# Kernel tuning notes

Hardware: AMD Instinct MI355X
Metric: run time of the kernel (lower is better)

Reference implementation:

```python
import jax, jax.numpy as jnp
import numpy as np

B, L, H = 32, 2048, 512


def setup_inputs() -> dict:
    key = jax.random.key(0)
    k1, k2, k3, k4, k5, k6 = jax.random.split(key, 6)
    scale = 1.0 / np.sqrt(H)
    return {
        "query": jax.random.normal(k1, (B, H), dtype=jnp.float32),
        "ref": jax.random.normal(k2, (B, L, H), dtype=jnp.float32),
        "mask": jax.random.randint(k3, (B, L), 0, 2) == 1,
        # learned params (torch Linear weight layout: [out, in]; apply as x @ W.T)
        "W_ref": jax.random.normal(k4, (H, H), dtype=jnp.float32) * scale,
        "W_q": jax.random.normal(k5, (H, H), dtype=jnp.float32) * scale,
        "v": jax.random.normal(k6, (H,), dtype=jnp.float32) * scale,
    }


def reference(query, ref, mask, W_ref, W_q, v):
    scale = 1.0 / np.sqrt(H)
    # additive (Bahdanau) scores: v^T tanh(W_ref ref + W_q q)
    encoded_ref = jnp.einsum("blh,oh->blo", ref, W_ref)          # (B, L, H)
    encoded_q = jnp.einsum("bh,oh->bo", query, W_q)[:, None, :]  # (B, 1, H)
    scores = jnp.einsum("blh,h->bl", jnp.tanh(encoded_ref + encoded_q), v)
    scores = scores * scale
    scores = jnp.where(mask, -1e9, scores)
    attn = jax.nn.softmax(scores, axis=1)                         # (B, L)
    glimpse = jnp.einsum("bl,blh->bh", attn, ref)                 # (B, H)
    return glimpse, scores
```

## Files before the change

### kernel.cpp

```cpp
#include <hip/hip_runtime.h>
#include <hip/hip_bf16.h>
#include <cstdint>

typedef __attribute__((ext_vector_type(4))) float f32x4;
typedef __attribute__((ext_vector_type(8))) short s16x8;

#define NB   32
#define NL   2048
#define NH   512
#define NM   (NB * NL)
#define SCALE 0.04419417382415922f

__device__ __forceinline__ ushort f2bf(float f) {
    __hip_bfloat16 b = __float2bfloat16(f);
    return *reinterpret_cast<ushort*>(&b);
}
__device__ __forceinline__ float bf2f(unsigned u) {
    union { unsigned u; float f; } a; a.u = u << 16; return a.f;
}
__device__ __forceinline__ unsigned long long pack4(float4 f) {
    union { ushort u[4]; unsigned long long v; } p;
    p.u[0] = f2bf(f.x); p.u[1] = f2bf(f.y); p.u[2] = f2bf(f.z); p.u[3] = f2bf(f.w);
    return p.v;
}

#define GL16(g, l)                                                         \
    __builtin_amdgcn_global_load_lds(                                      \
        (const __attribute__((address_space(1))) unsigned int*)(g),        \
        (__attribute__((address_space(3))) unsigned int*)(l), 16, 0, 0)

__global__ __launch_bounds__(256) void k_conv(const float* __restrict__ ref,
                                              ushort* __restrict__ refb,
                                              const float* __restrict__ W,
                                              ushort* __restrict__ Wb,
                                              const float* __restrict__ query,
                                              const float* __restrict__ Wq,
                                              float* __restrict__ eq) {
    int bid = blockIdx.x;
    int t = threadIdx.x;
    if (bid < 32768) {
        int g = bid * 256 + t;
        ((unsigned long long*)refb)[g] = pack4(((const float4*)ref)[g]);
    } else if (bid < 33024) {
        int g = (bid - 32768) * 256 + t;
        ((unsigned long long*)Wb)[g] = pack4(((const float4*)W)[g]);
    } else {
        __shared__ float q[NH];
        int b = bid - 33024;
        q[t] = query[b * NH + t];
        q[t + 256] = query[b * NH + t + 256];
        __syncthreads();
#pragma unroll
        for (int half = 0; half < 2; ++half) {
            int o = t + half * 256;
            const float4* w = (const float4*)(Wq + (size_t)o * NH);
            float acc = 0.f;
#pragma unroll 4
            for (int i = 0; i < NH / 4; ++i) {
                float4 x = w[i];
                acc += q[4 * i] * x.x + q[4 * i + 1] * x.y + q[4 * i + 2] * x.z + q[4 * i + 3] * x.w;
            }
            eq[b * NH + o] = acc;
        }
    }
}

__global__ __launch_bounds__(512, 1) void k_gemm8(const ushort* __restrict__ refb,
                                                  const ushort* __restrict__ Wb,
                                                  const float* __restrict__ eq,
                                                  const float* __restrict__ v,
                                                  float* __restrict__ part) {
    __shared__ ushort smem[65536];
    ushort* As0 = smem;
    ushort* Bs0 = smem + 16384;
    ushort* As1 = smem + 32768;
    ushort* Bs1 = smem + 49152;

    int tid = threadIdx.x;
    int lane = tid & 63, wid = tid >> 6;
    int wr = wid >> 2, wc = wid & 3;

    int phys = blockIdx.x;
    int xcd = phys & 7, slot = phys >> 3;
    int mt = xcd * 32 + (slot >> 1);
    int nt = slot & 1;
    int m0g = mt << 8, n0 = nt << 8;
    int b = mt >> 3;

    f32x4 acc[8][4];
#pragma unroll
    for (int i = 0; i < 8; ++i)
#pragma unroll
        for (int j = 0; j < 4; ++j) acc[i][j] = (f32x4)(0.f);

    int lr = lane & 15, kq = lane >> 4;
    int l7 = lr & 7;
    int sA0 = ((kq) ^ l7) << 3;
    int sA1 = ((4 + kq) ^ l7) << 3;
    int abase0 = (wr * 128 + lr) * 64;
    int bbase0 = (wc * 64 + lr) * 64;

#define STAGE(Asb, Bsb, kt)                                                    \
    {   _Pragma("unroll")                                                      \
        for (int ho = 0; ho < 4; ++ho) {                                       \
            int br = (ho >> 1) * 128 + wid * 16 + (ho & 1) * 8;                \
            int rl = br + (lane >> 3);                                         \
            int gc = (lane & 7) ^ (rl & 7);                                    \
            GL16(refb + (size_t)(m0g + rl) * NH + (kt) * 64 + gc * 8, (Asb) + br * 64); \
            GL16(Wb   + (size_t)(n0  + rl) * NH + (kt) * 64 + gc * 8, (Bsb) + br * 64); \
        } }

#define TILE_BODY(Asb, Bsb)                                                    \
    {   s16x8 bq[4][2];                                                        \
        _Pragma("unroll")                                                      \
        for (int fc = 0; fc < 4; ++fc) {                                       \
            bq[fc][0] = *(const s16x8*)&(Bsb)[bbase0 + fc * 1024 + sA0];       \
            bq[fc][1] = *(const s16x8*)&(Bsb)[bbase0 + fc * 1024 + sA1];       \
        }                                                                      \
        __builtin_amdgcn_s_setprio(1);                                         \
        _Pragma("unroll")                                                      \
        for (int fr = 0; fr < 8; ++fr) {                                       \
            s16x8 a0 = *(const s16x8*)&(Asb)[abase0 + fr * 1024 + sA0];        \
            s16x8 a1 = *(const s16x8*)&(Asb)[abase0 + fr * 1024 + sA1];        \
            _Pragma("unroll")                                                  \
            for (int fc = 0; fc < 4; ++fc) {                                   \
                acc[fr][fc] = __builtin_amdgcn_mfma_f32_16x16x32_bf16(         \
                    a0, bq[fc][0], acc[fr][fc], 0, 0, 0);                      \
                acc[fr][fc] = __builtin_amdgcn_mfma_f32_16x16x32_bf16(         \
                    a1, bq[fc][1], acc[fr][fc], 0, 0, 0);                      \
            }                                                                  \
        }                                                                      \
        __builtin_amdgcn_s_setprio(0);                                         \
    }

#define TILE(Asb, Bsb, WAITN, DOSTAGE, Asn, Bsn, kstage)                       \
    {   asm volatile("s_waitcnt vmcnt(" #WAITN ")" ::: "memory");              \
        __builtin_amdgcn_s_barrier();                                          \
        TILE_BODY(Asb, Bsb)                                                    \
        asm volatile("s_waitcnt lgkmcnt(0)" ::: "memory");                     \
        __builtin_amdgcn_s_barrier();                                          \
        if (DOSTAGE) STAGE(Asn, Bsn, kstage)                                   \
    }

    STAGE(As0, Bs0, 0)
    STAGE(As1, Bs1, 1)

    TILE(As0, Bs0, 8, 1, As0, Bs0, 2)
    TILE(As1, Bs1, 8, 1, As1, Bs1, 3)
    TILE(As0, Bs0, 8, 1, As0, Bs0, 4)
    TILE(As1, Bs1, 8, 1, As1, Bs1, 5)
    TILE(As0, Bs0, 8, 1, As0, Bs0, 6)
    TILE(As1, Bs1, 8, 1, As1, Bs1, 7)
    TILE(As0, Bs0, 8, 0, As0, Bs0, 0)
    TILE(As1, Bs1, 0, 0, As1, Bs1, 0)

#undef STAGE
#undef TILE_BODY
#undef TILE

    __syncthreads();

    float* sc_red = (float*)smem;
    const float* eqb = eq + b * NH;
    float vv[4], ee[4];
#pragma unroll
    for (int fc = 0; fc < 4; ++fc) {
        int c = n0 + wc * 64 + fc * 16 + lr;
        vv[fc] = v[c];
        ee[fc] = eqb[c];
    }
#pragma unroll
    for (int fr = 0; fr < 8; ++fr) {
#pragma unroll
        for (int reg = 0; reg < 4; ++reg) {
            float s = 0.f;
#pragma unroll
            for (int fc = 0; fc < 4; ++fc) {
                float x = acc[fr][fc][reg] + ee[fc];
                float t = 1.f - 2.f / (__expf(2.f * x) + 1.f);
                s += vv[fc] * t;
            }
            s += __shfl_xor(s, 1);
            s += __shfl_xor(s, 2);
            s += __shfl_xor(s, 4);
            s += __shfl_xor(s, 8);
            if (lr == 0) sc_red[wid * 128 + fr * 16 + kq * 4 + reg] = s;
        }
    }
    __syncthreads();
    if (tid < 256) {
        int row = tid;
        int g0 = (row >> 7) * 4;
        int rl = row & 127;
        float s = sc_red[(g0 + 0) * 128 + rl] + sc_red[(g0 + 1) * 128 + rl]
                + sc_red[(g0 + 2) * 128 + rl] + sc_red[(g0 + 3) * 128 + rl];
        part[(size_t)nt * NM + m0g + row] = s;
    }
}

__global__ __launch_bounds__(256) void k_smglp(const float* __restrict__ part,
                                               const int* __restrict__ mask,
                                               const ushort* __restrict__ refb,
                                               float* __restrict__ out_sc,
                                               float* __restrict__ glp) {
    int sp = blockIdx.x, b = blockIdx.y;
    int tid = threadIdx.x;
    int lane = tid & 63, wid = tid >> 6;
    __shared__ float red[4];
    __shared__ float asl[128];
    float sc[8];
    float mx = -3.4e38f;
#pragma unroll
    for (int i = 0; i < 8; ++i) {
        int m = b * NL + i * 256 + tid;
        float s = (part[m] + part[NM + m]) * SCALE;
        if (mask[m] != 0) s = -1e9f;
        if (sp == 0) out_sc[m] = s;
        sc[i] = s;
        mx = fmaxf(mx, s);
    }
#pragma unroll
    for (int o = 32; o >= 1; o >>= 1) mx = fmaxf(mx, __shfl_xor(mx, o));
    if (lane == 0) red[wid] = mx;
    __syncthreads();
    mx = fmaxf(fmaxf(red[0], red[1]), fmaxf(red[2], red[3]));
    __syncthreads();
    float ls = 0.f;
#pragma unroll
    for (int i = 0; i < 8; ++i) {
        float e = __expf(sc[i] - mx);
        ls += e;
        if (i == (sp >> 1) && (tid >> 7) == (sp & 1)) asl[tid & 127] = e;
    }
#pragma unroll
    for (int o = 32; o >= 1; o >>= 1) ls += __shfl_xor(ls, o);
    if (lane == 0) red[wid] = ls;
    __syncthreads();
    float inv = 1.f / (red[0] + red[1] + red[2] + red[3]);

    const ushort* rb = refb + ((size_t)b * NL + sp * 128) * NH;
    float2 acc = make_float2(0.f, 0.f);
#pragma unroll 4
    for (int l = 0; l < 128; ++l) {
        float a = asl[l];
        unsigned r = ((const unsigned*)(rb + (size_t)l * NH))[tid];
        acc.x += a * bf2f(r & 0xFFFFu);
        acc.y += a * bf2f(r >> 16);
    }
    acc.x *= inv;
    acc.y *= inv;
    ((float2*)(glp + (size_t)(sp * NB + b) * NH))[tid] = acc;
}

__global__ __launch_bounds__(256) void k_gred(const float* __restrict__ glp,
                                              float* __restrict__ out_gl) {
    int idx = blockIdx.x * 256 + threadIdx.x;
    float s = 0.f;
#pragma unroll
    for (int sp = 0; sp < 16; ++sp) s += glp[sp * (NB * NH) + idx];
    out_gl[idx] = s;
}

extern "C" void kernel_launch(void* const* d_in, const int* in_sizes, int n_in,
                              void* d_out, int out_size, void* d_ws, size_t ws_size,
                              hipStream_t stream) {
    const float* query = (const float*)d_in[0];
    const float* ref   = (const float*)d_in[1];
    const int*   mask  = (const int*)d_in[2];
    const float* W_ref = (const float*)d_in[3];
    const float* W_q   = (const float*)d_in[4];
    const float* v     = (const float*)d_in[5];

    float* out_gl = (float*)d_out;
    float* out_sc = out_gl + NB * NH;

    char* w = (char*)d_ws;
    ushort* wW   = (ushort*)w;
    float*  eq   = (float*)(w + 524288);
    ushort* refb = (ushort*)(w + 589824);
    float*  part = (float*)(w + 589824 + 67108864);
    float*  glp  = (float*)(w + 589824 + 67108864 + 524288);

    k_conv<<<33056, 256, 0, stream>>>(ref, refb, W_ref, wW, query, W_q, eq);
    k_gemm8<<<512, 512, 0, stream>>>(refb, wW, eq, v, part);
    k_smglp<<<dim3(16, NB), 256, 0, stream>>>(part, mask, refb, out_sc, glp);
    k_gred<<<64, 256, 0, stream>>>(glp, out_gl);
}
```

Baseline: 130.4 us.

## Fuse ref bf16 conversion into GEMM A-tile staging and read fp32 ref for glimpse

Drops the standalone pass that converted the full ref tensor to bf16. The GEMM now loads fp32 ref into registers, converts it, and writes swizzled bf16 into LDS while W tiles still use async global-to-LDS loads. The glimpse reduction reads fp32 ref directly. This removes a large write/read round trip through the workspace, at the cost of register-staged A loads with more VGPR pressure and doubled A bytes per GEMM load.

```diff
diff --git a/kernel.cpp b/kernel.cpp
--- a/kernel.cpp
+++ b/kernel.cpp
@@ -15,9 +15,6 @@
     __hip_bfloat16 b = __float2bfloat16(f);
     return *reinterpret_cast<ushort*>(&b);
 }
-__device__ __forceinline__ float bf2f(unsigned u) {
-    union { unsigned u; float f; } a; a.u = u << 16; return a.f;
-}
 __device__ __forceinline__ unsigned long long pack4(float4 f) {
     union { ushort u[4]; unsigned long long v; } p;
     p.u[0] = f2bf(f.x); p.u[1] = f2bf(f.y); p.u[2] = f2bf(f.z); p.u[3] = f2bf(f.w);
@@ -29,24 +26,25 @@
         (const __attribute__((address_space(1))) unsigned int*)(g),        \
         (__attribute__((address_space(3))) unsigned int*)(l), 16, 0, 0)
 
-__global__ __launch_bounds__(256) void k_conv(const float* __restrict__ ref,
-                                              ushort* __restrict__ refb,
-                                              const float* __restrict__ W,
-                                              ushort* __restrict__ Wb,
-                                              const float* __restrict__ query,
-                                              const float* __restrict__ Wq,
-                                              float* __restrict__ eq) {
+__global__ __launch_bounds__(256) void k_pre(const float* __restrict__ W,
+                                             ushort* __restrict__ Wb,
+                                             const float* __restrict__ query,
+                                             const float* __restrict__ Wq,
+                                             float* __restrict__ eq) {
     int bid = blockIdx.x;
     int t = threadIdx.x;
-    if (bid < 32768) {
-        int g = bid * 256 + t;
-        ((unsigned long long*)refb)[g] = pack4(((const float4*)ref)[g]);
-    } else if (bid < 33024) {
-        int g = (bid - 32768) * 256 + t;
-        ((unsigned long long*)Wb)[g] = pack4(((const float4*)W)[g]);
+    if (bid < 64) {
+        const float4* F = (const float4*)W;
+        unsigned long long* U = (unsigned long long*)Wb;
+        int base = bid * 1024 + t;
+        float4 f[4];
+#pragma unroll
+        for (int k = 0; k < 4; ++k) f[k] = F[base + k * 256];
+#pragma unroll
+        for (int k = 0; k < 4; ++k) U[base + k * 256] = pack4(f[k]);
     } else {
         __shared__ float q[NH];
-        int b = bid - 33024;
+        int b = bid - 64;
         q[t] = query[b * NH + t];
         q[t + 256] = query[b * NH + t + 256];
         __syncthreads();
@@ -65,7 +63,7 @@
     }
 }
 
-__global__ __launch_bounds__(512, 1) void k_gemm8(const ushort* __restrict__ refb,
+__global__ __launch_bounds__(512, 1) void k_gemm8(const float* __restrict__ ref,
                                                   const ushort* __restrict__ Wb,
                                                   const float* __restrict__ eq,
                                                   const float* __restrict__ v,
@@ -100,14 +98,30 @@
     int abase0 = (wr * 128 + lr) * 64;
     int bbase0 = (wc * 64 + lr) * 64;
 
-#define STAGE(Asb, Bsb, kt)                                                    \
+    const float* aglob = ref + (size_t)(m0g + wid * 32 + (lane >> 4)) * NH + (lane & 15) * 4;
+    float4 qa[8];
+
+#define STAGE_A(kt)                                                            \
+    {   _Pragma("unroll")                                                      \
+        for (int j = 0; j < 8; ++j)                                            \
+            qa[j] = *(const float4*)(aglob + (size_t)(j * 4) * NH + (kt) * 64); }
+
+#define WRITE_A(Asb)                                                           \
+    {   int s_ = lane & 15;                                                    \
+        _Pragma("unroll")                                                      \
+        for (int j = 0; j < 8; ++j) {                                          \
+            int rowj = wid * 32 + (lane >> 4) + j * 4;                         \
+            int idx = rowj * 64 + ((((s_ >> 1) ^ (rowj & 7))) << 3) + ((s_ & 1) << 2); \
+            *(unsigned long long*)&(Asb)[idx] = pack4(qa[j]);                  \
+        } }
+
+#define STAGE_B(Bsb, kt)                                                       \
     {   _Pragma("unroll")                                                      \
         for (int ho = 0; ho < 4; ++ho) {                                       \
-            int br = (ho >> 1) * 128 + wid * 16 + (ho & 1) * 8;                \
+            int br = wid * 32 + ho * 8;                                        \
             int rl = br + (lane >> 3);                                         \
             int gc = (lane & 7) ^ (rl & 7);                                    \
-            GL16(refb + (size_t)(m0g + rl) * NH + (kt) * 64 + gc * 8, (Asb) + br * 64); \
-            GL16(Wb   + (size_t)(n0  + rl) * NH + (kt) * 64 + gc * 8, (Bsb) + br * 64); \
+            GL16(Wb + (size_t)(n0 + rl) * NH + (kt) * 64 + gc * 8, (Bsb) + br * 64); \
         } }
 
 #define TILE_BODY(Asb, Bsb)                                                    \
@@ -133,30 +147,42 @@
         __builtin_amdgcn_s_setprio(0);                                         \
     }
 
-#define TILE(Asb, Bsb, WAITN, DOSTAGE, Asn, Bsn, kstage)                       \
-    {   asm volatile("s_waitcnt vmcnt(" #WAITN ")" ::: "memory");              \
-        __builtin_amdgcn_s_barrier();                                          \
-        TILE_BODY(Asb, Bsb)                                                    \
-        asm volatile("s_waitcnt lgkmcnt(0)" ::: "memory");                     \
-        __builtin_amdgcn_s_barrier();                                          \
-        if (DOSTAGE) STAGE(Asn, Bsn, kstage)                                   \
-    }
-
-    STAGE(As0, Bs0, 0)
-    STAGE(As1, Bs1, 1)
-
-    TILE(As0, Bs0, 8, 1, As0, Bs0, 2)
-    TILE(As1, Bs1, 8, 1, As1, Bs1, 3)
-    TILE(As0, Bs0, 8, 1, As0, Bs0, 4)
-    TILE(As1, Bs1, 8, 1, As1, Bs1, 5)
-    TILE(As0, Bs0, 8, 1, As0, Bs0, 6)
-    TILE(As1, Bs1, 8, 1, As1, Bs1, 7)
-    TILE(As0, Bs0, 8, 0, As0, Bs0, 0)
-    TILE(As1, Bs1, 0, 0, As1, Bs1, 0)
-
-#undef STAGE
+#define ENTRY(N)                                                               \
+    asm volatile("s_waitcnt lgkmcnt(0)" ::: "memory");                         \
+    asm volatile("s_waitcnt vmcnt(" #N ")" ::: "memory");                      \
+    __builtin_amdgcn_s_barrier();
+
+#define EXIT()                                                                 \
+    asm volatile("s_waitcnt lgkmcnt(0)" ::: "memory");                         \
+    __builtin_amdgcn_s_barrier();
+
+    STAGE_A(0) STAGE_B(Bs0, 0)
+    asm volatile("s_waitcnt vmcnt(4)" ::: "memory");
+    WRITE_A(As0)
+    STAGE_A(1) STAGE_B(Bs1, 1)
+
+    ENTRY(12) TILE_BODY(As0, Bs0) EXIT()
+    asm volatile("s_waitcnt vmcnt(4)" ::: "memory"); WRITE_A(As1) STAGE_A(2) STAGE_B(Bs0, 2)
+    ENTRY(12) TILE_BODY(As1, Bs1) EXIT()
+    asm volatile("s_waitcnt vmcnt(4)" ::: "memory"); WRITE_A(As0) STAGE_A(3) STAGE_B(Bs1, 3)
+    ENTRY(12) TILE_BODY(As0, Bs0) EXIT()
+    asm volatile("s_waitcnt vmcnt(4)" ::: "memory"); WRITE_A(As1) STAGE_A(4) STAGE_B(Bs0, 4)
+    ENTRY(12) TILE_BODY(As1, Bs1) EXIT()
+    asm volatile("s_waitcnt vmcnt(4)" ::: "memory"); WRITE_A(As0) STAGE_A(5) STAGE_B(Bs1, 5)
+    ENTRY(12) TILE_BODY(As0, Bs0) EXIT()
+    asm volatile("s_waitcnt vmcnt(4)" ::: "memory"); WRITE_A(As1) STAGE_A(6) STAGE_B(Bs0, 6)
+    ENTRY(12) TILE_BODY(As1, Bs1) EXIT()
+    asm volatile("s_waitcnt vmcnt(4)" ::: "memory"); WRITE_A(As0) STAGE_A(7) STAGE_B(Bs1, 7)
+    ENTRY(12) TILE_BODY(As0, Bs0) EXIT()
+    asm volatile("s_waitcnt vmcnt(4)" ::: "memory"); WRITE_A(As1)
+    ENTRY(0)  TILE_BODY(As1, Bs1)
+
+#undef STAGE_A
+#undef WRITE_A
+#undef STAGE_B
 #undef TILE_BODY
-#undef TILE
+#undef ENTRY
+#undef EXIT
 
     __syncthreads();
 
@@ -200,7 +226,7 @@
 
 __global__ __launch_bounds__(256) void k_smglp(const float* __restrict__ part,
                                                const int* __restrict__ mask,
-                                               const ushort* __restrict__ refb,
+                                               const float* __restrict__ ref,
                                                float* __restrict__ out_sc,
                                                float* __restrict__ glp) {
     int sp = blockIdx.x, b = blockIdx.y;
@@ -238,14 +264,14 @@
     __syncthreads();
     float inv = 1.f / (red[0] + red[1] + red[2] + red[3]);
 
-    const ushort* rb = refb + ((size_t)b * NL + sp * 128) * NH;
+    const float* rb = ref + ((size_t)b * NL + sp * 128) * NH;
     float2 acc = make_float2(0.f, 0.f);
 #pragma unroll 4
     for (int l = 0; l < 128; ++l) {
         float a = asl[l];
-        unsigned r = ((const unsigned*)(rb + (size_t)l * NH))[tid];
-        acc.x += a * bf2f(r & 0xFFFFu);
-        acc.y += a * bf2f(r >> 16);
+        float2 r = ((const float2*)(rb + (size_t)l * NH))[tid];
+        acc.x += a * r.x;
+        acc.y += a * r.y;
     }
     acc.x *= inv;
     acc.y *= inv;
@@ -277,12 +303,11 @@
     char* w = (char*)d_ws;
     ushort* wW   = (ushort*)w;
     float*  eq   = (float*)(w + 524288);
-    ushort* refb = (ushort*)(w + 589824);
-    float*  part = (float*)(w + 589824 + 67108864);
-    float*  glp  = (float*)(w + 589824 + 67108864 + 524288);
-
-    k_conv<<<33056, 256, 0, stream>>>(ref, refb, W_ref, wW, query, W_q, eq);
-    k_gemm8<<<512, 512, 0, stream>>>(refb, wW, eq, v, part);
-    k_smglp<<<dim3(16, NB), 256, 0, stream>>>(part, mask, refb, out_sc, glp);
+    float*  part = (float*)(w + 589824);
+    float*  glp  = (float*)(w + 1114112);
+
+    k_pre<<<96, 256, 0, stream>>>(W_ref, wW, query, W_q, eq);
+    k_gemm8<<<512, 512, 0, stream>>>(ref, wW, eq, v, part);
+    k_smglp<<<dim3(16, NB), 256, 0, stream>>>(part, mask, ref, out_sc, glp);
     k_gred<<<64, 256, 0, stream>>>(glp, out_gl);
 }
```

Result: slower. 178.9 us (+37.2%).
